# Kernel tuning notes

Measured on AMD Instinct MI355X. Metric: run time of the kernel, lower is better.

The kernel has to match this reference:

```python
import jax, jax.numpy as jnp
import numpy as np

B, N, M = 8, 8192, 2048
C1, C2 = 128, 256
H = 256  # mlp hidden/out channels


def setup_inputs() -> dict:
    key = jax.random.key(0)
    ks = jax.random.split(key, 8)
    return {
        "unknown": jax.random.normal(ks[0], (B, N, 3), dtype=jnp.float32),
        "known": jax.random.normal(ks[1], (B, M, 3), dtype=jnp.float32),
        "unknow_feats": jax.random.normal(ks[2], (B, C1, N), dtype=jnp.float32),
        "known_feats": jax.random.normal(ks[3], (B, C2, M), dtype=jnp.float32),
        "W1": jax.random.normal(ks[4], (H, C1 + C2), dtype=jnp.float32) * 0.02,
        "b1": jnp.zeros((H,), dtype=jnp.float32),
        "W2": jax.random.normal(ks[5], (H, H), dtype=jnp.float32) * 0.02,
        "b2": jnp.zeros((H,), dtype=jnp.float32),
    }


def _three_nn(unknown, known):
    # squared pairwise distances (B, n, m)
    d2 = jnp.sum((unknown[:, :, None, :] - known[:, None, :, :]) ** 2, axis=-1)
    neg_d2_top, idx = jax.lax.top_k(-d2, 3)  # 3 smallest distances
    dist = jnp.sqrt(jnp.maximum(-neg_d2_top, 0.0))  # (B, n, 3)
    return dist, idx


def _three_interpolate(features, idx, weight):
    # features: (B, c, m); idx, weight: (B, n, 3) -> (B, c, n)
    Bc, c, m = features.shape
    n = idx.shape[1]
    idx_flat = jnp.broadcast_to(idx.reshape(Bc, 1, n * 3), (Bc, c, n * 3))
    gathered = jnp.take_along_axis(features, idx_flat, axis=2).reshape(Bc, c, n, 3)
    return jnp.sum(gathered * weight[:, None, :, :], axis=-1)


def reference(unknown, known, unknow_feats, known_feats, W1, b1, W2, b2):
    dist, idx = _three_nn(unknown, known)
    dist_recip = 1.0 / (dist + 1e-8)
    weight = dist_recip / jnp.sum(dist_recip, axis=2, keepdims=True)  # (B, n, 3)
    interpolated = _three_interpolate(known_feats, idx, weight)  # (B, C2, n)
    new_features = jnp.concatenate([interpolated, unknow_feats], axis=1)  # (B, C1+C2, n)
    # shared MLP: two conv1x1 (bias, no BN) + ReLU
    h = jax.nn.relu(jnp.einsum('oc,bcn->bon', W1, new_features) + b1[None, :, None])
    out = jax.nn.relu(jnp.einsum('oc,bcn->bon', W2, h) + b2[None, :, None])
    return out
```

## Files before the change

### kernel.cpp

```cpp
#include <hip/hip_runtime.h>

using bf16x8 = __attribute__((ext_vector_type(8))) short;
using f32x4  = __attribute__((ext_vector_type(4))) float;

constexpr int Bb = 8, Nn = 8192, Mm = 2048, C1 = 128, C2 = 256, Hh = 256, K1 = 384;
constexpr int KT1 = K1 / 32;
constexpr int KT2 = Hh / 32;
constexpr int RT = Hh / 16;
constexpr int NQ = 4;
constexpr int MQ = Mm / NQ;

__device__ __forceinline__ short f2bf(float x) {
  union { float f; unsigned u; } v; v.f = x;
  unsigned r = v.u + 0x7fff + ((v.u >> 16) & 1);
  return (short)(r >> 16);
}

__device__ __forceinline__ void merge3(float a0, float a1, float a2, int A0, int A1, int A2,
                                       float b0, float b1, float b2, int B0, int B1, int B2,
                                       float& m0, float& m1, float& m2,
                                       int& j0, int& j1, int& j2) {
  bool ta = a0 <= b0;
  m0 = ta ? a0 : b0; j0 = ta ? A0 : B0;
  float na0 = ta ? a1 : a0, na1 = ta ? a2 : a1;
  int   nA0 = ta ? A1 : A0, nA1 = ta ? A2 : A1;
  float nb0 = ta ? b0 : b1, nb1 = ta ? b1 : b2;
  int   nB0 = ta ? B0 : B1, nB1 = ta ? B1 : B2;
  ta = na0 <= nb0;
  m1 = ta ? na0 : nb0; j1 = ta ? nA0 : nB0;
  float ma0 = ta ? na1 : na0; int mA0 = ta ? nA1 : nA0;
  float mb0 = ta ? nb0 : nb1; int mB0 = ta ? nB0 : nB1;
  ta = ma0 <= mb0;
  m2 = ta ? ma0 : mb0; j2 = ta ? mA0 : mB0;
}

__global__ __launch_bounds__(256) void prep_all_k(const float* __restrict__ kf,
                                                  float* __restrict__ kfT,
                                                  const float* __restrict__ W1,
                                                  const float* __restrict__ W2,
                                                  short* __restrict__ W1f,
                                                  short* __restrict__ W2f) {
  __shared__ float tile[32][33];
  int bid = blockIdx.x, tid = threadIdx.x;
  if (bid < 4096) {
    int cx = bid & 63, ry = (bid >> 6) & 7, z = bid >> 9;
    const int R = C2, C = Mm;
    const float* src = kf + (size_t)z * R * C;
    float* dst = kfT + (size_t)z * R * C;
    int c0 = cx * 32, r0 = ry * 32;
    int tx = tid & 31, ty = tid >> 5;
#pragma unroll
    for (int rr = ty; rr < 32; rr += 8) tile[rr][tx] = src[(size_t)(r0 + rr) * C + c0 + tx];
    __syncthreads();
#pragma unroll
    for (int cc = ty; cc < 32; cc += 8) dst[(size_t)(c0 + cc) * R + r0 + tx] = tile[tx][cc];
    return;
  }
  int id = (bid - 4096) * 256 + tid;
  const int n1 = KT1 * RT * 64;
  const int n2 = KT2 * RT * 64;
  if (id < n1) {
    int lane = id & 63, t = id >> 6;
    int kt = t / RT, rt = t % RT;
    int m = rt * 16 + (lane & 15), k0 = kt * 32 + (lane >> 4) * 8;
    bf16x8 f;
#pragma unroll
    for (int j = 0; j < 8; ++j) f[j] = f2bf(W1[(size_t)m * K1 + k0 + j]);
    *(bf16x8*)(W1f + (size_t)id * 8) = f;
  } else if (id < n1 + n2) {
    int id2 = id - n1;
    int lane = id2 & 63, t = id2 >> 6;
    int kt = t / RT, rt = t % RT;
    int m = rt * 16 + (lane & 15), k0 = kt * 32 + (lane >> 4) * 8;
    bf16x8 f;
#pragma unroll
    for (int j = 0; j < 8; ++j) f[j] = f2bf(W2[(size_t)m * Hh + k0 + j]);
    *(bf16x8*)(W2f + (size_t)id2 * 8) = f;
  }
}

__global__ __launch_bounds__(256) void nn_quarter_k(const float* __restrict__ unknown,
                                                    const float* __restrict__ known,
                                                    float* __restrict__ pd,
                                                    int* __restrict__ pi) {
  __shared__ float kx[MQ], ky[MQ], kz[MQ];
  int bid = blockIdx.x;
  int b = bid >> 7, rem = bid & 127;
  int q = rem & 3, nblk = rem >> 2;
  int n = nblk * 256 + threadIdx.x;
  const float* kb = known + ((size_t)b * Mm + q * MQ) * 3;
  for (int p = threadIdx.x; p < MQ; p += 256) {
    kx[p] = kb[3 * p]; ky[p] = kb[3 * p + 1]; kz[p] = kb[3 * p + 2];
  }
  __syncthreads();

  size_t ui = ((size_t)b * Nn + n) * 3;
  float ux = unknown[ui], uy = unknown[ui + 1], uz = unknown[ui + 2];
  float d0 = 1e30f, d1 = 1e30f, d2 = 1e30f;
  int i0 = 0, i1 = 0, i2 = 0;
  int gbase = q * MQ;

#define NN_STEP(xx, yy, zz, qq)                                         \
  {                                                                     \
    float dx = ux - (xx), dy = uy - (yy), dz = uz - (zz);               \
    float dd = dx * dx + dy * dy + dz * dz;                             \
    if (__any(dd < d2)) {    \
      int jm = gbase + jb + (qq);                                       \
      bool c0 = dd < d0, c1 = dd < d1, c2 = dd < d2;                    \
      d2 = c1 ? d1 : (c2 ? dd : d2); i2 = c1 ? i1 : (c2 ? jm : i2);     \
      d1 = c0 ? d0 : (c1 ? dd : d1); i1 = c0 ? i0 : (c1 ? jm : i1);     \
      d0 = c0 ? dd : d0;             i0 = c0 ? jm : i0;                 \
    }                                                                   \
  }

  for (int jb = 0; jb < MQ; jb += 4) {
    float4 xs = *(const float4*)&kx[jb];
    float4 ys = *(const float4*)&ky[jb];
    float4 zs = *(const float4*)&kz[jb];
    NN_STEP(xs.x, ys.x, zs.x, 0)
    NN_STEP(xs.y, ys.y, zs.y, 1)
    NN_STEP(xs.z, ys.z, zs.z, 2)
    NN_STEP(xs.w, ys.w, zs.w, 3)
  }
#undef NN_STEP

  size_t o = (((size_t)b * Nn + n) * NQ + q) * 3;
  pd[o] = d0; pd[o + 1] = d1; pd[o + 2] = d2;
  pi[o] = i0; pi[o + 1] = i1; pi[o + 2] = i2;
}

__global__ __launch_bounds__(256) void fused_gemm_k(
    const float* __restrict__ uf, const float* __restrict__ kfT,
    const short* __restrict__ W1f, const float* __restrict__ b1,
    const short* __restrict__ W2f, const float* __restrict__ b2,
    const float* __restrict__ pd, const int* __restrict__ pi,
    float* __restrict__ out) {
  __shared__ short Fs[KT1 * 4 * 64 * 8];
  __shared__ short Hs[KT2 * 4 * 64 * 8];
  int bid = blockIdx.x;
  int b = bid >> 7, bt = bid & 127;
  int tid = threadIdx.x, lane = tid & 63, wv = tid >> 6;
  int quad = lane >> 4, col = lane & 15;

  {
    int n = bt * 64 + wv * 16 + col;
    size_t pbase = (size_t)(b * Nn + n) * (NQ * 3);
    float4 da = *(const float4*)&pd[pbase];
    float4 db = *(const float4*)&pd[pbase + 4];
    float4 dc = *(const float4*)&pd[pbase + 8];
    int4 ia = *(const int4*)&pi[pbase];
    int4 ib = *(const int4*)&pi[pbase + 4];
    int4 ic = *(const int4*)&pi[pbase + 8];
    float t0, t1, t2, u0, u1, u2, m0, m1, m2;
    int T0, T1, T2, U0, U1, U2, g0, g1, g2;
    merge3(da.x, da.y, da.z, ia.x, ia.y, ia.z,
           da.w, db.x, db.y, ia.w, ib.x, ib.y, t0, t1, t2, T0, T1, T2);
    merge3(db.z, db.w, dc.x, ib.z, ib.w, ic.x,
           dc.y, dc.z, dc.w, ic.y, ic.z, ic.w, u0, u1, u2, U0, U1, U2);
    merge3(t0, t1, t2, T0, T1, T2, u0, u1, u2, U0, U1, U2,
           m0, m1, m2, g0, g1, g2);
    float s0 = sqrtf(m0), s1 = sqrtf(m1), s2 = sqrtf(m2);
    float r0 = 1.f / (s0 + 1e-8f), r1 = 1.f / (s1 + 1e-8f), r2 = 1.f / (s2 + 1e-8f);
    float rs = 1.f / (r0 + r1 + r2);
    float w0 = r0 * rs, w1 = r1 * rs, w2 = r2 * rs;

    const float* kfb = kfT + (size_t)b * Mm * C2;
#pragma unroll 2
    for (int kt = 0; kt < 8; ++kt) {
      int c0 = kt * 32 + quad * 8;
      float4 p0a = *(const float4*)&kfb[(size_t)g0 * C2 + c0];
      float4 p0b = *(const float4*)&kfb[(size_t)g0 * C2 + c0 + 4];
      float4 p1a = *(const float4*)&kfb[(size_t)g1 * C2 + c0];
      float4 p1b = *(const float4*)&kfb[(size_t)g1 * C2 + c0 + 4];
      float4 p2a = *(const float4*)&kfb[(size_t)g2 * C2 + c0];
      float4 p2b = *(const float4*)&kfb[(size_t)g2 * C2 + c0 + 4];
      bf16x8 f;
      f[0] = f2bf(w0 * p0a.x + w1 * p1a.x + w2 * p2a.x);
      f[1] = f2bf(w0 * p0a.y + w1 * p1a.y + w2 * p2a.y);
      f[2] = f2bf(w0 * p0a.z + w1 * p1a.z + w2 * p2a.z);
      f[3] = f2bf(w0 * p0a.w + w1 * p1a.w + w2 * p2a.w);
      f[4] = f2bf(w0 * p0b.x + w1 * p1b.x + w2 * p2b.x);
      f[5] = f2bf(w0 * p0b.y + w1 * p1b.y + w2 * p2b.y);
      f[6] = f2bf(w0 * p0b.z + w1 * p1b.z + w2 * p2b.z);
      f[7] = f2bf(w0 * p0b.w + w1 * p1b.w + w2 * p2b.w);
      *(bf16x8*)&Fs[((kt * 4 + wv) * 64 + lane) * 8] = f;
    }
#pragma unroll 2
    for (int kt = 8; kt < 12; ++kt) {
      int c1 = (kt - 8) * 32 + quad * 8;
      bf16x8 f;
#pragma unroll
      for (int j = 0; j < 8; ++j)
        f[j] = f2bf(uf[((size_t)b * C1 + c1 + j) * Nn + n]);
      *(bf16x8*)&Fs[((kt * 4 + wv) * 64 + lane) * 8] = f;
    }
  }
  __syncthreads();

  f32x4 acc[4][4];
#pragma unroll
  for (int r = 0; r < 4; ++r)
#pragma unroll
    for (int c = 0; c < 4; ++c) acc[r][c] = (f32x4){0.f, 0.f, 0.f, 0.f};

  for (int kt = 0; kt < KT1; ++kt) {
    bf16x8 Afr[4], Bfr[4];
#pragma unroll
    for (int r = 0; r < 4; ++r)
      Afr[r] = *(const bf16x8*)(W1f + ((size_t)(kt * RT + wv * 4 + r) * 64 + lane) * 8);
#pragma unroll
    for (int c = 0; c < 4; ++c)
      Bfr[c] = *(const bf16x8*)&Fs[((kt * 4 + c) * 64 + lane) * 8];
#pragma unroll
    for (int r = 0; r < 4; ++r)
#pragma unroll
      for (int c = 0; c < 4; ++c)
        acc[r][c] = __builtin_amdgcn_mfma_f32_16x16x32_bf16(Afr[r], Bfr[c], acc[r][c], 0, 0, 0);
  }

#pragma unroll
  for (int r = 0; r < 4; ++r) {
    f32x4 bq = *(const f32x4*)&b1[wv * 64 + r * 16 + quad * 4];
#pragma unroll
    for (int c = 0; c < 4; ++c)
#pragma unroll
      for (int reg = 0; reg < 4; ++reg)
        acc[r][c][reg] = fmaxf(acc[r][c][reg] + bq[reg], 0.f);
  }
  {
    int addr_lo = (((quad & 1) * 2) * 16 + col) * 4;
    bool hiSel = lane >= 32;
#pragma unroll
    for (int ktl = 0; ktl < 2; ++ktl)
#pragma unroll
      for (int c = 0; c < 4; ++c) {
        bf16x8 f;
#pragma unroll
        for (int j = 0; j < 8; ++j) {
          int addr = addr_lo + (j >> 2) * 64;
          int lo = __builtin_amdgcn_ds_bpermute(addr, __float_as_int(acc[ktl * 2][c][j & 3]));
          int hi = __builtin_amdgcn_ds_bpermute(addr, __float_as_int(acc[ktl * 2 + 1][c][j & 3]));
          f[j] = f2bf(__int_as_float(hiSel ? hi : lo));
        }
        *(bf16x8*)&Hs[(((wv * 2 + ktl) * 4 + c) * 64 + lane) * 8] = f;
      }
  }
  __syncthreads();

  f32x4 acc2[4][4];
#pragma unroll
  for (int r = 0; r < 4; ++r)
#pragma unroll
    for (int c = 0; c < 4; ++c) acc2[r][c] = (f32x4){0.f, 0.f, 0.f, 0.f};

  for (int kt = 0; kt < KT2; ++kt) {
    bf16x8 Afr[4], Bfr[4];
#pragma unroll
    for (int r = 0; r < 4; ++r)
      Afr[r] = *(const bf16x8*)(W2f + ((size_t)(kt * RT + wv * 4 + r) * 64 + lane) * 8);
#pragma unroll
    for (int c = 0; c < 4; ++c)
      Bfr[c] = *(const bf16x8*)&Hs[((kt * 4 + c) * 64 + lane) * 8];
#pragma unroll
    for (int r = 0; r < 4; ++r)
#pragma unroll
      for (int c = 0; c < 4; ++c)
        acc2[r][c] = __builtin_amdgcn_mfma_f32_16x16x32_bf16(Afr[r], Bfr[c], acc2[r][c], 0, 0, 0);
  }

#pragma unroll
  for (int r = 0; r < 4; ++r) {
    f32x4 bq = *(const f32x4*)&b2[wv * 64 + r * 16 + quad * 4];
#pragma unroll
    for (int c = 0; c < 4; ++c)
#pragma unroll
      for (int reg = 0; reg < 4; ++reg) {
        int rowg = wv * 64 + r * 16 + quad * 4 + reg;
        int n = bt * 64 + c * 16 + col;
        out[((size_t)b * Hh + rowg) * Nn + n] = fmaxf(acc2[r][c][reg] + bq[reg], 0.f);
      }
  }
}

extern "C" void kernel_launch(void* const* d_in, const int* in_sizes, int n_in,
                              void* d_out, int out_size, void* d_ws, size_t ws_size,
                              hipStream_t stream) {
  const float* unknown = (const float*)d_in[0];
  const float* known   = (const float*)d_in[1];
  const float* uf      = (const float*)d_in[2];
  const float* kf      = (const float*)d_in[3];
  const float* W1      = (const float*)d_in[4];
  const float* b1      = (const float*)d_in[5];
  const float* W2      = (const float*)d_in[6];
  const float* b2      = (const float*)d_in[7];
  float* out = (float*)d_out;

  char* p = (char*)d_ws;
  float* kfT = (float*)p;  p += (size_t)Bb * Mm * C2 * 4;
  short* W1f = (short*)p;  p += (size_t)KT1 * RT * 64 * 8 * 2;
  short* W2f = (short*)p;  p += (size_t)KT2 * RT * 64 * 8 * 2;
  float* pd  = (float*)p;  p += (size_t)Bb * Nn * NQ * 3 * 4;
  int* pi    = (int*)p;    p += (size_t)Bb * Nn * NQ * 3 * 4;

  const int prep_blocks = 4096 + (KT1 * RT * 64 + KT2 * RT * 64 + 255) / 256;
  prep_all_k<<<dim3(prep_blocks), dim3(256), 0, stream>>>(kf, kfT, W1, W2, W1f, W2f);
  nn_quarter_k<<<dim3(Bb * 32 * NQ), dim3(256), 0, stream>>>(unknown, known, pd, pi);
  fused_gemm_k<<<dim3(Bb * (Nn / 64)), dim3(256), 0, stream>>>(
      uf, kfT, W1f, b1, W2f, b2, pd, pi, out);
}
```

Measured before the change: 223.5 us.

## Merge nearest-neighbor search into prep kernel and read known points via scalar loads

Folds the three-NN search blocks into the same launch as the feature transpose and weight packing, removing one kernel launch and letting the independent work overlap. The NN loop drops its LDS staging and syncthreads and instead reads known coordinates through wave-uniform addresses (readfirstlane) so they can become scalar loads. The gather loop in the fused GEMM kernel is also unrolled further. Risks: scalar-load latency in the tight NN loop, and NN blocks being scheduled behind the many transpose blocks in the combined grid.

```diff
diff --git a/kernel.cpp b/kernel.cpp
--- a/kernel.cpp
+++ b/kernel.cpp
@@ -9,6 +9,11 @@
 constexpr int RT = Hh / 16;
 constexpr int NQ = 4;
 constexpr int MQ = Mm / NQ;
+
+constexpr int TR_BLOCKS = 4096;
+constexpr int WP_BLOCKS = (KT1 * RT * 64 + KT2 * RT * 64) / 256;
+constexpr int NN_BASE   = TR_BLOCKS + WP_BLOCKS;
+constexpr int NN_BLOCKS = Bb * 32 * NQ;
 
 __device__ __forceinline__ short f2bf(float x) {
   union { float f; unsigned u; } v; v.f = x;
@@ -34,15 +39,20 @@
   m2 = ta ? ma0 : mb0; j2 = ta ? mA0 : mB0;
 }
 
-__global__ __launch_bounds__(256) void prep_all_k(const float* __restrict__ kf,
-                                                  float* __restrict__ kfT,
-                                                  const float* __restrict__ W1,
-                                                  const float* __restrict__ W2,
-                                                  short* __restrict__ W1f,
-                                                  short* __restrict__ W2f) {
+__global__ __launch_bounds__(256) void prep_nn_k(const float* __restrict__ kf,
+                                                 float* __restrict__ kfT,
+                                                 const float* __restrict__ W1,
+                                                 const float* __restrict__ W2,
+                                                 short* __restrict__ W1f,
+                                                 short* __restrict__ W2f,
+                                                 const float* __restrict__ unknown,
+                                                 const float* __restrict__ known,
+                                                 float* __restrict__ pd,
+                                                 int* __restrict__ pi) {
   __shared__ float tile[32][33];
   int bid = blockIdx.x, tid = threadIdx.x;
-  if (bid < 4096) {
+
+  if (bid < TR_BLOCKS) {
     int cx = bid & 63, ry = (bid >> 6) & 7, z = bid >> 9;
     const int R = C2, C = Mm;
     const float* src = kf + (size_t)z * R * C;
@@ -56,49 +66,44 @@
     for (int cc = ty; cc < 32; cc += 8) dst[(size_t)(c0 + cc) * R + r0 + tx] = tile[tx][cc];
     return;
   }
-  int id = (bid - 4096) * 256 + tid;
-  const int n1 = KT1 * RT * 64;
-  const int n2 = KT2 * RT * 64;
-  if (id < n1) {
-    int lane = id & 63, t = id >> 6;
-    int kt = t / RT, rt = t % RT;
-    int m = rt * 16 + (lane & 15), k0 = kt * 32 + (lane >> 4) * 8;
-    bf16x8 f;
-#pragma unroll
-    for (int j = 0; j < 8; ++j) f[j] = f2bf(W1[(size_t)m * K1 + k0 + j]);
-    *(bf16x8*)(W1f + (size_t)id * 8) = f;
-  } else if (id < n1 + n2) {
-    int id2 = id - n1;
-    int lane = id2 & 63, t = id2 >> 6;
-    int kt = t / RT, rt = t % RT;
-    int m = rt * 16 + (lane & 15), k0 = kt * 32 + (lane >> 4) * 8;
-    bf16x8 f;
-#pragma unroll
-    for (int j = 0; j < 8; ++j) f[j] = f2bf(W2[(size_t)m * Hh + k0 + j]);
-    *(bf16x8*)(W2f + (size_t)id2 * 8) = f;
-  }
-}
-
-__global__ __launch_bounds__(256) void nn_quarter_k(const float* __restrict__ unknown,
-                                                    const float* __restrict__ known,
-                                                    float* __restrict__ pd,
-                                                    int* __restrict__ pi) {
-  __shared__ float kx[MQ], ky[MQ], kz[MQ];
-  int bid = blockIdx.x;
-  int b = bid >> 7, rem = bid & 127;
-  int q = rem & 3, nblk = rem >> 2;
-  int n = nblk * 256 + threadIdx.x;
-  const float* kb = known + ((size_t)b * Mm + q * MQ) * 3;
-  for (int p = threadIdx.x; p < MQ; p += 256) {
-    kx[p] = kb[3 * p]; ky[p] = kb[3 * p + 1]; kz[p] = kb[3 * p + 2];
-  }
-  __syncthreads();
-
-  size_t ui = ((size_t)b * Nn + n) * 3;
-  float ux = unknown[ui], uy = unknown[ui + 1], uz = unknown[ui + 2];
-  float d0 = 1e30f, d1 = 1e30f, d2 = 1e30f;
-  int i0 = 0, i1 = 0, i2 = 0;
-  int gbase = q * MQ;
+
+  if (bid < NN_BASE) {
+    int id = (bid - TR_BLOCKS) * 256 + tid;
+    const int n1 = KT1 * RT * 64;
+    const int n2 = KT2 * RT * 64;
+    if (id < n1) {
+      int lane = id & 63, t = id >> 6;
+      int kt = t / RT, rt = t % RT;
+      int m = rt * 16 + (lane & 15), k0 = kt * 32 + (lane >> 4) * 8;
+      bf16x8 f;
+#pragma unroll
+      for (int j = 0; j < 8; ++j) f[j] = f2bf(W1[(size_t)m * K1 + k0 + j]);
+      *(bf16x8*)(W1f + (size_t)id * 8) = f;
+    } else if (id < n1 + n2) {
+      int id2 = id - n1;
+      int lane = id2 & 63, t = id2 >> 6;
+      int kt = t / RT, rt = t % RT;
+      int m = rt * 16 + (lane & 15), k0 = kt * 32 + (lane >> 4) * 8;
+      bf16x8 f;
+#pragma unroll
+      for (int j = 0; j < 8; ++j) f[j] = f2bf(W2[(size_t)m * Hh + k0 + j]);
+      *(bf16x8*)(W2f + (size_t)id2 * 8) = f;
+    }
+    return;
+  }
+
+  {
+    int bidn = bid - NN_BASE;
+    int b = bidn >> 7, rem = bidn & 127;
+    int q = rem & 3, nblk = rem >> 2;
+    int n = nblk * 256 + tid;
+    const float* kb = known + ((size_t)b * Mm + q * MQ) * 3;
+
+    size_t ui = ((size_t)b * Nn + n) * 3;
+    float ux = unknown[ui], uy = unknown[ui + 1], uz = unknown[ui + 2];
+    float d0 = 1e30f, d1 = 1e30f, d2 = 1e30f;
+    int i0 = 0, i1 = 0, i2 = 0;
+    int gbase = q * MQ;
 
 #define NN_STEP(xx, yy, zz, qq)                                         \
   {                                                                     \
@@ -113,20 +118,24 @@
     }                                                                   \
   }
 
-  for (int jb = 0; jb < MQ; jb += 4) {
-    float4 xs = *(const float4*)&kx[jb];
-    float4 ys = *(const float4*)&ky[jb];
-    float4 zs = *(const float4*)&kz[jb];
-    NN_STEP(xs.x, ys.x, zs.x, 0)
-    NN_STEP(xs.y, ys.y, zs.y, 1)
-    NN_STEP(xs.z, ys.z, zs.z, 2)
-    NN_STEP(xs.w, ys.w, zs.w, 3)
-  }
+    for (int jb = 0; jb < MQ; jb += 4) {
+      int jbu = __builtin_amdgcn_readfirstlane(jb);
+      const float* kq = kb + 3 * (size_t)jbu;
+      float k0x = kq[0], k0y = kq[1],  k0z = kq[2];
+      float k1x = kq[3], k1y = kq[4],  k1z = kq[5];
+      float k2x = kq[6], k2y = kq[7],  k2z = kq[8];
+      float k3x = kq[9], k3y = kq[10], k3z = kq[11];
+      NN_STEP(k0x, k0y, k0z, 0)
+      NN_STEP(k1x, k1y, k1z, 1)
+      NN_STEP(k2x, k2y, k2z, 2)
+      NN_STEP(k3x, k3y, k3z, 3)
+    }
 #undef NN_STEP
 
-  size_t o = (((size_t)b * Nn + n) * NQ + q) * 3;
-  pd[o] = d0; pd[o + 1] = d1; pd[o + 2] = d2;
-  pi[o] = i0; pi[o + 1] = i1; pi[o + 2] = i2;
+    size_t o = (((size_t)b * Nn + n) * NQ + q) * 3;
+    pd[o] = d0; pd[o + 1] = d1; pd[o + 2] = d2;
+    pi[o] = i0; pi[o + 1] = i1; pi[o + 2] = i2;
+  }
 }
 
 __global__ __launch_bounds__(256) void fused_gemm_k(
@@ -165,7 +174,7 @@
     float w0 = r0 * rs, w1 = r1 * rs, w2 = r2 * rs;
 
     const float* kfb = kfT + (size_t)b * Mm * C2;
-#pragma unroll 2
+#pragma unroll 4
     for (int kt = 0; kt < 8; ++kt) {
       int c0 = kt * 32 + quad * 8;
       float4 p0a = *(const float4*)&kfb[(size_t)g0 * C2 + c0];
@@ -302,9 +311,8 @@
   float* pd  = (float*)p;  p += (size_t)Bb * Nn * NQ * 3 * 4;
   int* pi    = (int*)p;    p += (size_t)Bb * Nn * NQ * 3 * 4;
 
-  const int prep_blocks = 4096 + (KT1 * RT * 64 + KT2 * RT * 64 + 255) / 256;
-  prep_all_k<<<dim3(prep_blocks), dim3(256), 0, stream>>>(kf, kfT, W1, W2, W1f, W2f);
-  nn_quarter_k<<<dim3(Bb * 32 * NQ), dim3(256), 0, stream>>>(unknown, known, pd, pi);
+  prep_nn_k<<<dim3(NN_BASE + NN_BLOCKS), dim3(256), 0, stream>>>(
+      kf, kfT, W1, W2, W1f, W2f, unknown, known, pd, pi);
   fused_gemm_k<<<dim3(Bb * (Nn / 64)), dim3(256), 0, stream>>>(
       uf, kfT, W1f, b1, W2f, b2, pd, pi, out);
 }
```

New measurement: 254.9 us. +14.0%, slower.
